# Kernel tuning notes

Measured on AMD Instinct MI355X. Metric: run time of the kernel, lower is better.

Reference implementation:

```python
import jax, jax.numpy as jnp
import numpy as np

N_NODES = 50000   # local subgraph nodes
N_ENT   = 100000  # global entity vocab
N_REL   = 16
DIM     = 128
LAYERS  = 2
E       = 600000  # edges
Q       = 8192    # query triples
PATH_DIM = 5
RULE_INIT = [[1.0, 1.0, 0.5, 0.0, 0.0], [0.0, 0.0, 0.0, 1.0, 1.0]]


def setup_inputs() -> dict:
    key = jax.random.key(0)
    ks = jax.random.split(key, 11)
    node_ids   = jax.random.randint(ks[0], (N_NODES,), 0, N_ENT)
    edge_index = jax.random.randint(ks[1], (2, E), 0, N_NODES)
    edge_type  = jax.random.randint(ks[2], (E,), 0, N_REL)
    heads = jax.random.randint(ks[3], (Q,), 0, N_NODES)
    rels  = jax.random.randint(ks[4], (Q,), 0, N_REL)
    tails = jax.random.randint(ks[5], (Q,), 0, N_NODES)
    path_feat = jax.random.normal(ks[6], (Q, PATH_DIM), dtype=jnp.float32)
    # learned parameters
    entity_emb = jax.random.normal(ks[7], (N_ENT, DIM), dtype=jnp.float32) * 0.1
    rel_emb    = jax.random.normal(ks[8], (N_REL, DIM), dtype=jnp.float32) * 0.1
    W_self = jax.random.normal(ks[9], (LAYERS, DIM, DIM), dtype=jnp.float32) / np.sqrt(DIM)
    W_rel  = jax.random.normal(ks[10], (LAYERS, N_REL, DIM, DIM), dtype=jnp.float32) / np.sqrt(DIM)
    delta_weight = jnp.zeros((2, PATH_DIM), dtype=jnp.float32)
    lambda_logit = jnp.zeros((2,), dtype=jnp.float32)
    rule_init_weight = jnp.asarray(RULE_INIT, dtype=jnp.float32)
    return {
        'node_ids': node_ids, 'edge_index': edge_index, 'edge_type': edge_type,
        'heads': heads, 'rels': rels, 'tails': tails,
        'path_feat': path_feat, 'rel_task_idx': 0,
        'entity_emb': entity_emb, 'rel_emb': rel_emb,
        'W_self': W_self, 'W_rel': W_rel,
        'delta_weight': delta_weight, 'lambda_logit': lambda_logit,
        'rule_init_weight': rule_init_weight,
    }


def _rgcn_layer(h, Ws, Wr, src, dst, etype):
    # relation-specific transforms for all nodes: [R, N, D]
    h_rel = jnp.einsum('nd,rde->rne', h, Wr)
    msgs = h_rel[etype, src]                    # [E, D] gather per edge
    # per-(dst, relation) mean normalization (standard RGCN 1/c_{i,r})
    seg = dst * N_REL + etype
    cnt = jax.ops.segment_sum(jnp.ones((E,), h.dtype), seg, num_segments=N_NODES * N_REL)
    msgs = msgs / jnp.maximum(cnt[seg], 1.0)[:, None]
    agg = jax.ops.segment_sum(msgs, dst, num_segments=N_NODES)  # [N, D]
    return jax.nn.relu(h @ Ws + agg)


def reference(node_ids, edge_index, edge_type, heads, rels, tails, path_feat,
              rel_task_idx, entity_emb, rel_emb, W_self, W_rel,
              delta_weight, lambda_logit, rule_init_weight):
    src, dst = edge_index[0], edge_index[1]
    h = entity_emb[node_ids]                      # [N, D] local node states
    for l in range(LAYERS):
        h = _rgcn_layer(h, W_self[l], W_rel[l], src, dst, edge_type)
    # DistMult scoring of query triples (local indices)
    score_graph = jnp.sum(h[heads] * rel_emb[rels] * h[tails], axis=-1)  # [Q]
    # path branch
    final_weight = rule_init_weight[rel_task_idx] + delta_weight[rel_task_idx]  # [PATH_DIM]
    score_path = path_feat @ final_weight                                # [Q]
    lam = jax.nn.sigmoid(lambda_logit[rel_task_idx])
    return lam * score_graph + (1.0 - lam) * score_path
```

## Files before the change

kernel.cpp:

```cpp
#include <hip/hip_runtime.h>

#define N_NODES 50000
#define N_ENT   100000
#define N_REL   16
#define DIM     128
#define E_EDGES 600000
#define NQ      8192
#define PATH_DIM 5
#define NK      (N_NODES * N_REL)
#define KTOT    (N_REL * DIM + DIM)
#define NG      (KTOT / 32)
#define BM      64

typedef __attribute__((ext_vector_type(8))) short short8;
typedef __attribute__((ext_vector_type(4))) float floatx4;

static __device__ __forceinline__ short f2bf(float x) {
  unsigned u = __builtin_bit_cast(unsigned, x);
  u = (u + 0x7FFFu + ((u >> 16) & 1u)) >> 16;
  return (short)u;
}
static __device__ __forceinline__ float bf_lo(unsigned u) {
  return __builtin_bit_cast(float, u << 16);
}
static __device__ __forceinline__ float bf_hi(unsigned u) {
  return __builtin_bit_cast(float, u & 0xffff0000u);
}
static __device__ __forceinline__ unsigned pk2(float a, float b) {
  return (unsigned)(unsigned short)f2bf(a) | ((unsigned)(unsigned short)f2bf(b) << 16);
}

__global__ void k_bucket(const int* __restrict__ ei, const int* __restrict__ et,
                         int* __restrict__ cnt, int* __restrict__ head,
                         int* __restrict__ cursor, int* __restrict__ slots,
                         int* __restrict__ ovf_src, int* __restrict__ ovf_next) {
  int e = blockIdx.x * 256 + threadIdx.x;
  if (e >= E_EDGES) return;
  int src = ei[e];
  int key = et[e] * N_NODES + ei[E_EDGES + e];
  int pos = atomicAdd(&cnt[key], 1);
  if (pos < 4) {
    slots[(size_t)key * 4 + pos] = src;
  } else {
    int nid = atomicAdd(cursor, 1) + 1;
    ovf_src[nid] = src;
    ovf_next[nid] = atomicExch(&head[key], nid);
  }
}

__global__ void k_h0(const int* __restrict__ nid, const float* __restrict__ emb,
                     unsigned* __restrict__ h) {
  int g = blockIdx.x * 256 + threadIdx.x;
  int n = g >> 5;
  int q = g & 31;
  float4 v = *(const float4*)(emb + (size_t)nid[n] * DIM + q * 4);
  uint2 pk;
  pk.x = pk2(v.x, v.y);
  pk.y = pk2(v.z, v.w);
  *(uint2*)(h + (size_t)n * 64 + q * 2) = pk;
}

__global__ void k_wcat(const float* __restrict__ wrel, const float* __restrict__ wself,
                       short* __restrict__ wt) {
  int idx = blockIdx.x * 256 + threadIdx.x;
  if (idx >= 2 * NG * 8 * 512) return;
  int within = idx & 511;
  int tile = idx >> 9;
  int rA = within >> 5, q = within & 31;
  int nt8 = tile & 7;
  int lg = tile >> 3;
  int l = lg / NG, g = lg % NG;
  int n = nt8 * 16 + rA;
  int k = g * 32 + q;
  float v;
  if (k < N_REL * DIM) {
    int r = k >> 7, d = k & 127;
    v = wrel[(((size_t)l * N_REL + r) * DIM + d) * DIM + n];
  } else {
    int d = k - N_REL * DIM;
    v = wself[((size_t)l * DIM + d) * DIM + n];
  }
  wt[idx] = f2bf(v);
}

__global__ __launch_bounds__(512, 4) void k_layer(const unsigned* __restrict__ hin,
                                                  const int* __restrict__ gcnt,
                                                  const int* __restrict__ slots,
                                                  const int* __restrict__ head,
                                                  const int* __restrict__ ovf_src,
                                                  const int* __restrict__ ovf_next,
                                                  const short* __restrict__ wt,
                                                  const unsigned* __restrict__ zrow,
                                                  unsigned* __restrict__ hout) {
  __shared__ unsigned As[2][BM][68];
  int t = threadIdx.x;
  int w = t >> 6, lane = t & 63;
  int row0 = blockIdx.x * BM;

  if (w < 4) {
    int pw = w;
    int seg = lane & 15, edge = lane >> 4;
    int segbase = row0 + pw * 16;
    int k0 = min(segbase + seg, NK - 1);
    int cl  = gcnt[k0];
    int pfe = slots[(size_t)k0 * 4 + edge];

    auto produce = [&](int buf, int it) {
      float invl = 1.0f / (float)(cl > 0 ? cl : 1);
      int invb = __builtin_bit_cast(int, invl);
      unsigned u0[16], u1[16], u2[16], u3[16];
      #pragma unroll
      for (int j = 0; j < 16; ++j) {
        int cj = __builtin_amdgcn_readlane(cl, j);
        if (cj > 0) {
          int r0 = __builtin_amdgcn_readlane(pfe, j);
          int r1 = __builtin_amdgcn_readlane(pfe, j + 16);
          int r2 = __builtin_amdgcn_readlane(pfe, j + 32);
          int r3 = __builtin_amdgcn_readlane(pfe, j + 48);
          const unsigned* p1 = (cj > 1) ? hin + (size_t)r1 * 64 : zrow;
          const unsigned* p2 = (cj > 2) ? hin + (size_t)r2 * 64 : zrow;
          const unsigned* p3 = (cj > 3) ? hin + (size_t)r3 * 64 : zrow;
          u0[j] = hin[(size_t)r0 * 64 + lane];
          u1[j] = p1[lane];
          u2[j] = p2[lane];
          u3[j] = p3[lane];
        }
      }
      int cl_n = 0, pfe_n = 0;
      if (it < 15) {
        int kn = min((it + 1) * N_NODES + segbase + seg, NK - 1);
        cl_n = gcnt[kn];
        pfe_n = slots[(size_t)kn * 4 + edge];
      }
      __builtin_amdgcn_sched_barrier(0);
      #pragma unroll
      for (int j = 0; j < 16; ++j) {
        int cj = __builtin_amdgcn_readlane(cl, j);
        if (cj == 0) {
          As[buf][pw * 16 + j][lane] = 0u;
        } else {
          float inv = __builtin_bit_cast(float, __builtin_amdgcn_readlane(invb, j));
          float s0 = bf_lo(u0[j]) + bf_lo(u1[j]) + bf_lo(u2[j]) + bf_lo(u3[j]);
          float s1 = bf_hi(u0[j]) + bf_hi(u1[j]) + bf_hi(u2[j]) + bf_hi(u3[j]);
          if (cj > 4) {
            int kj = min(it * N_NODES + segbase + j, NK - 1);
            int cur = __builtin_amdgcn_readfirstlane(head[kj]);
            for (int x = 4; x < cj; ++x) {
              int sr = __builtin_amdgcn_readfirstlane(ovf_src[cur]);
              unsigned uu = hin[(size_t)sr * 64 + lane];
              s0 += bf_lo(uu); s1 += bf_hi(uu);
              cur = __builtin_amdgcn_readfirstlane(ovf_next[cur]);
            }
          }
          s0 *= inv; s1 *= inv;
          unsigned pk;
          asm("v_cvt_pk_bf16_f32 %0, %1, %2" : "=v"(pk) : "v"(s0), "v"(s1));
          As[buf][pw * 16 + j][lane] = pk;
        }
      }
      cl = cl_n; pfe = pfe_n;
    };

    produce(0, 0);
    __syncthreads();
    for (int it = 0; it < 17; ++it) {
      int nx = it + 1;
      if (nx < 16) {
        produce(nx & 1, nx);
      } else if (nx == 16) {
        #pragma unroll
        for (int j = 0; j < 16; ++j) {
          int lr = min(segbase + j, N_NODES - 1);
          As[0][pw * 16 + j][lane] = hin[(size_t)lr * 64 + lane];
        }
      }
      __syncthreads();
    }
  } else {
    int wid = w - 4, wm = wid >> 1, wn = wid & 1;
    int quad = lane >> 4, rA = lane & 15;
    floatx4 acc[2][4];
    #pragma unroll
    for (int a = 0; a < 2; a++)
      #pragma unroll
      for (int b = 0; b < 4; b++) acc[a][b] = (floatx4)0.f;

    __syncthreads();
    for (int it = 0; it < 17; ++it) {
      int buf = it & 1;
      const short* arow0 = (const short*)&As[buf][wm * 32 + rA][0];
      const short* arow1 = (const short*)&As[buf][wm * 32 + 16 + rA][0];
      #pragma unroll
      for (int ks = 0; ks < 4; ++ks) {
        short8 a0 = *(const short8*)(arow0 + ks * 32 + quad * 8);
        short8 a1 = *(const short8*)(arow1 + ks * 32 + quad * 8);
        int kg = it * 4 + ks;
        const short* bp = wt + (size_t)(kg * 8 + wn * 4) * 512 + rA * 32 + quad * 8;
        #pragma unroll
        for (int nt = 0; nt < 4; ++nt) {
          short8 b = *(const short8*)(bp + nt * 512);
          acc[0][nt] = __builtin_amdgcn_mfma_f32_16x16x32_bf16(a0, b, acc[0][nt], 0, 0, 0);
          acc[1][nt] = __builtin_amdgcn_mfma_f32_16x16x32_bf16(a1, b, acc[1][nt], 0, 0, 0);
        }
      }
      __syncthreads();
    }
    #pragma unroll
    for (int mt = 0; mt < 2; ++mt)
      #pragma unroll
      for (int nt = 0; nt < 4; ++nt)
        #pragma unroll
        for (int j = 0; j < 4; ++j) {
          int row = row0 + wm * 32 + mt * 16 + quad * 4 + j;
          int col = wn * 64 + nt * 16 + rA;
          if (row < N_NODES)
            ((short*)hout)[(size_t)row * DIM + col] = f2bf(fmaxf(acc[mt][nt][j], 0.f));
        }
  }
}

__global__ void k_score(const unsigned* __restrict__ h, const int* __restrict__ heads,
                        const int* __restrict__ rels, const int* __restrict__ tails,
                        const float* __restrict__ rel_emb, const float* __restrict__ path_feat,
                        const int* __restrict__ task_idx, const float* __restrict__ delta_w,
                        const float* __restrict__ lambda_logit, const float* __restrict__ rule_init,
                        float* __restrict__ out) {
  int q = (blockIdx.x * 256 + threadIdx.x) >> 6;
  int lane = threadIdx.x & 63;
  int hd = heads[q], tl = tails[q], rl = rels[q];
  unsigned ua = h[(size_t)hd * 64 + lane];
  unsigned uc = h[(size_t)tl * 64 + lane];
  float2 r = *(const float2*)(rel_emb + (size_t)rl * DIM + lane * 2);
  float s = bf_lo(ua) * r.x * bf_lo(uc) + bf_hi(ua) * r.y * bf_hi(uc);
  #pragma unroll
  for (int off = 32; off; off >>= 1) s += __shfl_xor(s, off, 64);
  if (lane == 0) {
    int task = task_idx[0];
    float sp = 0.f;
    #pragma unroll
    for (int p = 0; p < PATH_DIM; p++)
      sp += path_feat[q * PATH_DIM + p] *
            (rule_init[task * PATH_DIM + p] + delta_w[task * PATH_DIM + p]);
    float lam = 1.f / (1.f + __expf(-lambda_logit[task]));
    out[q] = lam * s + (1.f - lam) * sp;
  }
}

extern "C" void kernel_launch(void* const* d_in, const int* in_sizes, int n_in,
                              void* d_out, int out_size, void* d_ws, size_t ws_size,
                              hipStream_t stream) {
  const int*   node_ids   = (const int*)d_in[0];
  const int*   edge_index = (const int*)d_in[1];
  const int*   edge_type  = (const int*)d_in[2];
  const int*   heads      = (const int*)d_in[3];
  const int*   rels       = (const int*)d_in[4];
  const int*   tails      = (const int*)d_in[5];
  const float* path_feat  = (const float*)d_in[6];
  const int*   task_idx   = (const int*)d_in[7];
  const float* entity_emb = (const float*)d_in[8];
  const float* rel_emb    = (const float*)d_in[9];
  const float* W_self     = (const float*)d_in[10];
  const float* W_rel      = (const float*)d_in[11];
  const float* delta_w    = (const float*)d_in[12];
  const float* lambda_lg  = (const float*)d_in[13];
  const float* rule_init  = (const float*)d_in[14];

  char* ws = (char*)d_ws;
  size_t off = 0;
  auto alloc = [&](size_t bytes) -> void* {
    void* p = ws + off;
    off = (off + bytes + 255) & ~(size_t)255;
    return p;
  };
  unsigned* h_a    = (unsigned*)alloc((size_t)N_NODES * DIM * 2);
  unsigned* h_b    = (unsigned*)alloc((size_t)N_NODES * DIM * 2);
  short*    wt     = (short*)alloc((size_t)2 * NG * 8 * 512 * 2);
  int*      zreg   = (int*)alloc((size_t)(2 * NK + 64) * 4);
  int*      cntA   = zreg;
  int*      headA  = zreg + NK;
  int*      cursor = zreg + 2 * NK;
  int*      slots  = (int*)alloc((size_t)NK * 4 * 4);
  int*      ovf_s  = (int*)alloc((size_t)(E_EDGES + 2) * 4);
  int*      ovf_n  = (int*)alloc((size_t)(E_EDGES + 2) * 4);
  unsigned* zrow   = (unsigned*)alloc(256);

  hipMemsetAsync(zreg, 0, (size_t)(2 * NK + 64) * 4, stream);
  hipMemsetAsync(zrow, 0, 256, stream);
  int eb = (E_EDGES + 255) / 256;
  k_bucket<<<eb, 256, 0, stream>>>(edge_index, edge_type, cntA, headA, cursor,
                                   slots, ovf_s, ovf_n);
  k_h0<<<(N_NODES * 32) / 256, 256, 0, stream>>>(node_ids, entity_emb, h_a);
  k_wcat<<<(2 * NG * 8 * 512 + 255) / 256, 256, 0, stream>>>(W_rel, W_self, wt);

  const unsigned* hin = h_a;
  unsigned* hout = h_b;
  int nblk = (N_NODES + BM - 1) / BM;
  for (int l = 0; l < 2; l++) {
    k_layer<<<nblk, 512, 0, stream>>>(hin, cntA, slots, headA, ovf_s, ovf_n,
                                      wt + (size_t)l * NG * 8 * 512, zrow, hout);
    const unsigned* tmp = hout;
    hout = (unsigned*)hin;
    hin = tmp;
  }
  k_score<<<NQ / 4, 256, 0, stream>>>(hin, heads, rels, tails, rel_emb, path_feat,
                                      task_idx, delta_w, lambda_lg, rule_init,
                                      (float*)d_out);
}
```

Measured before the change: 508.3 us.

## Unify producer/consumer waves in layer kernel with software-pipelined gathers and fused prep

The layer kernel no longer splits waves into gather producers and MFMA consumers. All 8 waves now gather neighbor rows and run MFMA, using inline-asm global loads and explicit vmcnt waits, so weight fetches and the next batch of gathers overlap the current matmul. The three setup kernels (bucket, h0, weight cast) are merged into one launch, and the zero-row memset is folded into the main memset. This should raise concurrency and cut launch overhead, but it depends on fragile manual waitcnt accounting and on higher register pressure.

```diff
diff --git a/kernel.cpp b/kernel.cpp
--- a/kernel.cpp
+++ b/kernel.cpp
@@ -11,6 +11,9 @@
 #define KTOT    (N_REL * DIM + DIM)
 #define NG      (KTOT / 32)
 #define BM      64
+#define EB      ((E_EDGES + 255) / 256)
+#define H0B     ((N_NODES * 32) / 256)
+#define WCB     ((2 * NG * 8 * 512) / 256)
 
 typedef __attribute__((ext_vector_type(8))) short short8;
 typedef __attribute__((ext_vector_type(4))) float floatx4;
@@ -30,193 +33,219 @@
   return (unsigned)(unsigned short)f2bf(a) | ((unsigned)(unsigned short)f2bf(b) << 16);
 }
 
-__global__ void k_bucket(const int* __restrict__ ei, const int* __restrict__ et,
-                         int* __restrict__ cnt, int* __restrict__ head,
-                         int* __restrict__ cursor, int* __restrict__ slots,
-                         int* __restrict__ ovf_src, int* __restrict__ ovf_next) {
-  int e = blockIdx.x * 256 + threadIdx.x;
-  if (e >= E_EDGES) return;
-  int src = ei[e];
-  int key = et[e] * N_NODES + ei[E_EDGES + e];
-  int pos = atomicAdd(&cnt[key], 1);
-  if (pos < 4) {
-    slots[(size_t)key * 4 + pos] = src;
+static __device__ __forceinline__ unsigned gload_u(const unsigned* p) {
+  unsigned r;
+  asm volatile("global_load_dword %0, %1, off" : "=v"(r) : "v"(p) : "memory");
+  return r;
+}
+static __device__ __forceinline__ int gload_s(const int* p) {
+  int r;
+  asm volatile("global_load_dword %0, %1, off" : "=v"(r) : "v"(p) : "memory");
+  return r;
+}
+static __device__ __forceinline__ short8 gload_b(const short* p) {
+  short8 r;
+  asm volatile("global_load_dwordx4 %0, %1, off" : "=v"(r) : "v"(p) : "memory");
+  return r;
+}
+#define WAIT_VM(N) do { asm volatile("s_waitcnt vmcnt(" #N ")" ::: "memory"); \
+                        __builtin_amdgcn_sched_barrier(0); } while (0)
+
+__global__ void k_prep(const int* __restrict__ ei, const int* __restrict__ et,
+                       int* __restrict__ cnt, int* __restrict__ head,
+                       int* __restrict__ cursor, int* __restrict__ slots,
+                       int* __restrict__ ovf_src, int* __restrict__ ovf_next,
+                       const int* __restrict__ nid, const float* __restrict__ emb,
+                       unsigned* __restrict__ h,
+                       const float* __restrict__ wrel, const float* __restrict__ wself,
+                       short* __restrict__ wt) {
+  int b = blockIdx.x, t = threadIdx.x;
+  if (b < EB) {
+    int e = b * 256 + t;
+    if (e < E_EDGES) {
+      int src = ei[e];
+      int key = et[e] * N_NODES + ei[E_EDGES + e];
+      int pos = atomicAdd(&cnt[key], 1);
+      if (pos < 4) {
+        slots[(size_t)key * 4 + pos] = src;
+      } else {
+        int nid2 = atomicAdd(cursor, 1) + 1;
+        ovf_src[nid2] = src;
+        ovf_next[nid2] = atomicExch(&head[key], nid2);
+      }
+    }
+  } else if (b < EB + H0B) {
+    int g = (b - EB) * 256 + t;
+    int n = g >> 5, q = g & 31;
+    float4 v = *(const float4*)(emb + (size_t)nid[n] * DIM + q * 4);
+    uint2 pk;
+    pk.x = pk2(v.x, v.y);
+    pk.y = pk2(v.z, v.w);
+    *(uint2*)(h + (size_t)n * 64 + q * 2) = pk;
   } else {
-    int nid = atomicAdd(cursor, 1) + 1;
-    ovf_src[nid] = src;
-    ovf_next[nid] = atomicExch(&head[key], nid);
-  }
-}
-
-__global__ void k_h0(const int* __restrict__ nid, const float* __restrict__ emb,
-                     unsigned* __restrict__ h) {
-  int g = blockIdx.x * 256 + threadIdx.x;
-  int n = g >> 5;
-  int q = g & 31;
-  float4 v = *(const float4*)(emb + (size_t)nid[n] * DIM + q * 4);
-  uint2 pk;
-  pk.x = pk2(v.x, v.y);
-  pk.y = pk2(v.z, v.w);
-  *(uint2*)(h + (size_t)n * 64 + q * 2) = pk;
-}
-
-__global__ void k_wcat(const float* __restrict__ wrel, const float* __restrict__ wself,
-                       short* __restrict__ wt) {
-  int idx = blockIdx.x * 256 + threadIdx.x;
-  if (idx >= 2 * NG * 8 * 512) return;
-  int within = idx & 511;
-  int tile = idx >> 9;
-  int rA = within >> 5, q = within & 31;
-  int nt8 = tile & 7;
-  int lg = tile >> 3;
-  int l = lg / NG, g = lg % NG;
-  int n = nt8 * 16 + rA;
-  int k = g * 32 + q;
-  float v;
-  if (k < N_REL * DIM) {
-    int r = k >> 7, d = k & 127;
-    v = wrel[(((size_t)l * N_REL + r) * DIM + d) * DIM + n];
-  } else {
-    int d = k - N_REL * DIM;
-    v = wself[((size_t)l * DIM + d) * DIM + n];
-  }
-  wt[idx] = f2bf(v);
-}
-
-__global__ __launch_bounds__(512, 4) void k_layer(const unsigned* __restrict__ hin,
-                                                  const int* __restrict__ gcnt,
-                                                  const int* __restrict__ slots,
-                                                  const int* __restrict__ head,
-                                                  const int* __restrict__ ovf_src,
-                                                  const int* __restrict__ ovf_next,
-                                                  const short* __restrict__ wt,
-                                                  const unsigned* __restrict__ zrow,
-                                                  unsigned* __restrict__ hout) {
+    int idx = (b - EB - H0B) * 256 + t;
+    int within = idx & 511;
+    int tile = idx >> 9;
+    int rA = within >> 5, q = within & 31;
+    int nt8 = tile & 7;
+    int lg = tile >> 3;
+    int l = lg / NG, g = lg % NG;
+    int n = nt8 * 16 + rA;
+    int k = g * 32 + q;
+    float v;
+    if (k < N_REL * DIM) {
+      int r = k >> 7, d = k & 127;
+      v = wrel[(((size_t)l * N_REL + r) * DIM + d) * DIM + n];
+    } else {
+      int d = k - N_REL * DIM;
+      v = wself[((size_t)l * DIM + d) * DIM + n];
+    }
+    wt[idx] = f2bf(v);
+  }
+}
+
+__global__ __attribute__((amdgpu_flat_work_group_size(512, 512),
+                          amdgpu_waves_per_eu(2, 4)))
+void k_layer(const unsigned* __restrict__ hin, const int* __restrict__ gcnt,
+             const int* __restrict__ slots, const int* __restrict__ head,
+             const int* __restrict__ ovf_src, const int* __restrict__ ovf_next,
+             const short* __restrict__ wt, const unsigned* __restrict__ zrow,
+             unsigned* __restrict__ hout) {
   __shared__ unsigned As[2][BM][68];
   int t = threadIdx.x;
   int w = t >> 6, lane = t & 63;
+  int quad = lane >> 4, rA = lane & 15;
+  int wm = w >> 2, wn = w & 3;
   int row0 = blockIdx.x * BM;
-
-  if (w < 4) {
-    int pw = w;
-    int seg = lane & 15, edge = lane >> 4;
-    int segbase = row0 + pw * 16;
-    int k0 = min(segbase + seg, NK - 1);
-    int cl  = gcnt[k0];
-    int pfe = slots[(size_t)k0 * 4 + edge];
-
-    auto produce = [&](int buf, int it) {
-      float invl = 1.0f / (float)(cl > 0 ? cl : 1);
-      int invb = __builtin_bit_cast(int, invl);
-      unsigned u0[16], u1[16], u2[16], u3[16];
+  int segbase = row0 + w * 8;
+  int lpi = lane & 31, segp = lpi & 7, edgep = lpi >> 3;
+
+  floatx4 acc[2][2];
+  #pragma unroll
+  for (int a = 0; a < 2; a++)
+    #pragma unroll
+    for (int c = 0; c < 2; c++) acc[a][c] = (floatx4)0.f;
+
+  unsigned u0[8], u1[8], u2[8], u3[8];
+  short8 bf[4][2];
+  int cl, pfe, cl_n, pfe_n;
+
+  auto issue_batch = [&]() {
+    #pragma unroll
+    for (int j = 0; j < 8; ++j) {
+      int cj = __builtin_amdgcn_readlane(cl, j);
+      int r0 = __builtin_amdgcn_readlane(pfe, j);
+      int r1 = __builtin_amdgcn_readlane(pfe, j + 8);
+      int r2 = __builtin_amdgcn_readlane(pfe, j + 16);
+      int r3 = __builtin_amdgcn_readlane(pfe, j + 24);
+      u0[j] = gload_u(((cj > 0) ? hin + (size_t)r0 * 64 : zrow) + lane);
+      u1[j] = gload_u(((cj > 1) ? hin + (size_t)r1 * 64 : zrow) + lane);
+      u2[j] = gload_u(((cj > 2) ? hin + (size_t)r2 * 64 : zrow) + lane);
+      u3[j] = gload_u(((cj > 3) ? hin + (size_t)r3 * 64 : zrow) + lane);
+    }
+  };
+  auto issue_cp = [&](int itn) {
+    int keyn = min(itn * N_NODES + segbase + segp, NK - 1);
+    cl_n  = gload_s(gcnt + keyn);
+    pfe_n = gload_s(slots + (size_t)keyn * 4 + edgep);
+  };
+  auto issue_b = [&](int rr) {
+    #pragma unroll
+    for (int ks = 0; ks < 4; ++ks)
       #pragma unroll
-      for (int j = 0; j < 16; ++j) {
-        int cj = __builtin_amdgcn_readlane(cl, j);
-        if (cj > 0) {
-          int r0 = __builtin_amdgcn_readlane(pfe, j);
-          int r1 = __builtin_amdgcn_readlane(pfe, j + 16);
-          int r2 = __builtin_amdgcn_readlane(pfe, j + 32);
-          int r3 = __builtin_amdgcn_readlane(pfe, j + 48);
-          const unsigned* p1 = (cj > 1) ? hin + (size_t)r1 * 64 : zrow;
-          const unsigned* p2 = (cj > 2) ? hin + (size_t)r2 * 64 : zrow;
-          const unsigned* p3 = (cj > 3) ? hin + (size_t)r3 * 64 : zrow;
-          u0[j] = hin[(size_t)r0 * 64 + lane];
-          u1[j] = p1[lane];
-          u2[j] = p2[lane];
-          u3[j] = p3[lane];
+      for (int ntl = 0; ntl < 2; ++ntl)
+        bf[ks][ntl] = gload_b(wt + (size_t)((rr * 4 + ks) * 8 + wn * 2 + ntl) * 512
+                                  + rA * 32 + quad * 8);
+  };
+  auto do_mfma = [&](int rr) {
+    int buf = rr & 1;
+    #pragma unroll
+    for (int ks = 0; ks < 4; ++ks) {
+      short8 a0 = *(const short8*)((const short*)&As[buf][wm * 32 + rA][0] + ks * 32 + quad * 8);
+      short8 a1 = *(const short8*)((const short*)&As[buf][wm * 32 + 16 + rA][0] + ks * 32 + quad * 8);
+      #pragma unroll
+      for (int ntl = 0; ntl < 2; ++ntl) {
+        acc[0][ntl] = __builtin_amdgcn_mfma_f32_16x16x32_bf16(a0, bf[ks][ntl], acc[0][ntl], 0, 0, 0);
+        acc[1][ntl] = __builtin_amdgcn_mfma_f32_16x16x32_bf16(a1, bf[ks][ntl], acc[1][ntl], 0, 0, 0);
+      }
+    }
+  };
+  auto accum = [&](int it, int buf) {
+    float invl = 1.0f / (float)(cl > 0 ? cl : 1);
+    int invb = __builtin_bit_cast(int, invl);
+    #pragma unroll
+    for (int j = 0; j < 8; ++j) {
+      int cj = __builtin_amdgcn_readlane(cl, j);
+      float inv = __builtin_bit_cast(float, __builtin_amdgcn_readlane(invb, j));
+      float s0 = bf_lo(u0[j]) + bf_lo(u1[j]) + bf_lo(u2[j]) + bf_lo(u3[j]);
+      float s1 = bf_hi(u0[j]) + bf_hi(u1[j]) + bf_hi(u2[j]) + bf_hi(u3[j]);
+      if (cj > 4) {
+        int kj = min(it * N_NODES + segbase + j, NK - 1);
+        int cur = __builtin_amdgcn_readfirstlane(head[kj]);
+        for (int x = 4; x < cj; ++x) {
+          int sr = __builtin_amdgcn_readfirstlane(ovf_src[cur]);
+          unsigned uu = hin[(size_t)sr * 64 + lane];
+          s0 += bf_lo(uu); s1 += bf_hi(uu);
+          cur = __builtin_amdgcn_readfirstlane(ovf_next[cur]);
         }
       }
-      int cl_n = 0, pfe_n = 0;
-      if (it < 15) {
-        int kn = min((it + 1) * N_NODES + segbase + seg, NK - 1);
-        cl_n = gcnt[kn];
-        pfe_n = slots[(size_t)kn * 4 + edge];
+      s0 *= inv; s1 *= inv;
+      unsigned pk;
+      asm("v_cvt_pk_bf16_f32 %0, %1, %2" : "=v"(pk) : "v"(s0), "v"(s1));
+      As[buf][w * 8 + j][lane] = pk;
+    }
+  };
+
+  {
+    int key0 = min(segbase + segp, NK - 1);
+    cl  = gcnt[key0];
+    pfe = slots[(size_t)key0 * 4 + edgep];
+  }
+  issue_batch();
+  issue_cp(1);
+  WAIT_VM(0);
+  accum(0, 0);
+  __syncthreads();
+  cl = cl_n; pfe = pfe_n;
+
+  for (int it = 1; it <= 15; ++it) {
+    issue_b(it - 1);
+    issue_batch();
+    issue_cp(it + 1);
+    WAIT_VM(34);
+    do_mfma(it - 1);
+    WAIT_VM(0);
+    accum(it, it & 1);
+    __syncthreads();
+    cl = cl_n; pfe = pfe_n;
+  }
+
+  issue_b(15);
+  #pragma unroll
+  for (int j = 0; j < 8; ++j)
+    u0[j] = gload_u(hin + (size_t)min(segbase + j, N_NODES - 1) * 64 + lane);
+  WAIT_VM(8);
+  do_mfma(15);
+  WAIT_VM(0);
+  #pragma unroll
+  for (int j = 0; j < 8; ++j) As[0][w * 8 + j][lane] = u0[j];
+  __syncthreads();
+
+  issue_b(16);
+  WAIT_VM(0);
+  do_mfma(16);
+
+  #pragma unroll
+  for (int mt = 0; mt < 2; ++mt)
+    #pragma unroll
+    for (int ntl = 0; ntl < 2; ++ntl)
+      #pragma unroll
+      for (int j = 0; j < 4; ++j) {
+        int row = row0 + wm * 32 + mt * 16 + quad * 4 + j;
+        int col = wn * 32 + ntl * 16 + rA;
+        if (row < N_NODES)
+          ((short*)hout)[(size_t)row * DIM + col] = f2bf(fmaxf(acc[mt][ntl][j], 0.f));
       }
-      __builtin_amdgcn_sched_barrier(0);
-      #pragma unroll
-      for (int j = 0; j < 16; ++j) {
-        int cj = __builtin_amdgcn_readlane(cl, j);
-        if (cj == 0) {
-          As[buf][pw * 16 + j][lane] = 0u;
-        } else {
-          float inv = __builtin_bit_cast(float, __builtin_amdgcn_readlane(invb, j));
-          float s0 = bf_lo(u0[j]) + bf_lo(u1[j]) + bf_lo(u2[j]) + bf_lo(u3[j]);
-          float s1 = bf_hi(u0[j]) + bf_hi(u1[j]) + bf_hi(u2[j]) + bf_hi(u3[j]);
-          if (cj > 4) {
-            int kj = min(it * N_NODES + segbase + j, NK - 1);
-            int cur = __builtin_amdgcn_readfirstlane(head[kj]);
-            for (int x = 4; x < cj; ++x) {
-              int sr = __builtin_amdgcn_readfirstlane(ovf_src[cur]);
-              unsigned uu = hin[(size_t)sr * 64 + lane];
-              s0 += bf_lo(uu); s1 += bf_hi(uu);
-              cur = __builtin_amdgcn_readfirstlane(ovf_next[cur]);
-            }
-          }
-          s0 *= inv; s1 *= inv;
-          unsigned pk;
-          asm("v_cvt_pk_bf16_f32 %0, %1, %2" : "=v"(pk) : "v"(s0), "v"(s1));
-          As[buf][pw * 16 + j][lane] = pk;
-        }
-      }
-      cl = cl_n; pfe = pfe_n;
-    };
-
-    produce(0, 0);
-    __syncthreads();
-    for (int it = 0; it < 17; ++it) {
-      int nx = it + 1;
-      if (nx < 16) {
-        produce(nx & 1, nx);
-      } else if (nx == 16) {
-        #pragma unroll
-        for (int j = 0; j < 16; ++j) {
-          int lr = min(segbase + j, N_NODES - 1);
-          As[0][pw * 16 + j][lane] = hin[(size_t)lr * 64 + lane];
-        }
-      }
-      __syncthreads();
-    }
-  } else {
-    int wid = w - 4, wm = wid >> 1, wn = wid & 1;
-    int quad = lane >> 4, rA = lane & 15;
-    floatx4 acc[2][4];
-    #pragma unroll
-    for (int a = 0; a < 2; a++)
-      #pragma unroll
-      for (int b = 0; b < 4; b++) acc[a][b] = (floatx4)0.f;
-
-    __syncthreads();
-    for (int it = 0; it < 17; ++it) {
-      int buf = it & 1;
-      const short* arow0 = (const short*)&As[buf][wm * 32 + rA][0];
-      const short* arow1 = (const short*)&As[buf][wm * 32 + 16 + rA][0];
-      #pragma unroll
-      for (int ks = 0; ks < 4; ++ks) {
-        short8 a0 = *(const short8*)(arow0 + ks * 32 + quad * 8);
-        short8 a1 = *(const short8*)(arow1 + ks * 32 + quad * 8);
-        int kg = it * 4 + ks;
-        const short* bp = wt + (size_t)(kg * 8 + wn * 4) * 512 + rA * 32 + quad * 8;
-        #pragma unroll
-        for (int nt = 0; nt < 4; ++nt) {
-          short8 b = *(const short8*)(bp + nt * 512);
-          acc[0][nt] = __builtin_amdgcn_mfma_f32_16x16x32_bf16(a0, b, acc[0][nt], 0, 0, 0);
-          acc[1][nt] = __builtin_amdgcn_mfma_f32_16x16x32_bf16(a1, b, acc[1][nt], 0, 0, 0);
-        }
-      }
-      __syncthreads();
-    }
-    #pragma unroll
-    for (int mt = 0; mt < 2; ++mt)
-      #pragma unroll
-      for (int nt = 0; nt < 4; ++nt)
-        #pragma unroll
-        for (int j = 0; j < 4; ++j) {
-          int row = row0 + wm * 32 + mt * 16 + quad * 4 + j;
-          int col = wn * 64 + nt * 16 + rA;
-          if (row < N_NODES)
-            ((short*)hout)[(size_t)row * DIM + col] = f2bf(fmaxf(acc[mt][nt][j], 0.f));
-        }
-  }
 }
 
 __global__ void k_score(const unsigned* __restrict__ h, const int* __restrict__ heads,
@@ -275,22 +304,20 @@
   unsigned* h_a    = (unsigned*)alloc((size_t)N_NODES * DIM * 2);
   unsigned* h_b    = (unsigned*)alloc((size_t)N_NODES * DIM * 2);
   short*    wt     = (short*)alloc((size_t)2 * NG * 8 * 512 * 2);
-  int*      zreg   = (int*)alloc((size_t)(2 * NK + 64) * 4);
+  int*      zreg   = (int*)alloc((size_t)(2 * NK + 128) * 4);
   int*      cntA   = zreg;
   int*      headA  = zreg + NK;
   int*      cursor = zreg + 2 * NK;
+  unsigned* zrow   = (unsigned*)(zreg + 2 * NK + 64);
   int*      slots  = (int*)alloc((size_t)NK * 4 * 4);
   int*      ovf_s  = (int*)alloc((size_t)(E_EDGES + 2) * 4);
   int*      ovf_n  = (int*)alloc((size_t)(E_EDGES + 2) * 4);
-  unsigned* zrow   = (unsigned*)alloc(256);
-
-  hipMemsetAsync(zreg, 0, (size_t)(2 * NK + 64) * 4, stream);
-  hipMemsetAsync(zrow, 0, 256, stream);
-  int eb = (E_EDGES + 255) / 256;
-  k_bucket<<<eb, 256, 0, stream>>>(edge_index, edge_type, cntA, headA, cursor,
-                                   slots, ovf_s, ovf_n);
-  k_h0<<<(N_NODES * 32) / 256, 256, 0, stream>>>(node_ids, entity_emb, h_a);
-  k_wcat<<<(2 * NG * 8 * 512 + 255) / 256, 256, 0, stream>>>(W_rel, W_self, wt);
+
+  hipMemsetAsync(zreg, 0, (size_t)(2 * NK + 128) * 4, stream);
+  k_prep<<<EB + H0B + WCB, 256, 0, stream>>>(edge_index, edge_type, cntA, headA,
+                                             cursor, slots, ovf_s, ovf_n,
+                                             node_ids, entity_emb, h_a,
+                                             W_rel, W_self, wt);
 
   const unsigned* hin = h_a;
   unsigned* hout = h_b;
```

Result: no change. 516.8 us (+1.7%).
